# Kernel tuning notes

Measured on AMD Instinct MI355X. Metric: run time of the kernel, lower is better.

## Reference

```python
import jax, jax.numpy as jnp
import numpy as np

HIDDEN_DIM = 1024
HEAD_DIM = 64


def setup_inputs() -> dict:
    key = jax.random.key(0)
    kx, kq, kk, kv, ko = jax.random.split(key, 5)
    B, S = 4, 4096
    x = jax.random.normal(kx, (B, S, HIDDEN_DIM), dtype=jnp.float32)
    # nn.Linear(in, out, bias=False) weight has shape [out, in]; y = x @ W.T
    scale = 1.0 / np.sqrt(HIDDEN_DIM)
    Wq = jax.random.normal(kq, (HEAD_DIM, HIDDEN_DIM), dtype=jnp.float32) * scale
    Wk = jax.random.normal(kk, (HEAD_DIM, HIDDEN_DIM), dtype=jnp.float32) * scale
    Wv = jax.random.normal(kv, (HEAD_DIM, HIDDEN_DIM), dtype=jnp.float32) * scale
    Wo = jax.random.normal(ko, (HIDDEN_DIM, HEAD_DIM), dtype=jnp.float32) * (1.0 / np.sqrt(HEAD_DIM))
    return {"x": x, "Wq": Wq, "Wk": Wk, "Wv": Wv, "Wo": Wo}


def reference(x, Wq, Wk, Wv, Wo):
    # projections: x [B,S,H] @ W.T [H,D] -> [B,S,D]
    q = jnp.einsum('bsh,dh->bsd', x, Wq)
    k = jnp.einsum('bsh,dh->bsd', x, Wk)
    v = jnp.einsum('bsh,dh->bsd', x, Wv)
    d = q.shape[-1]
    scores = jnp.einsum('bqd,bkd->bqk', q, k) / jnp.sqrt(jnp.asarray(d, q.dtype))
    S = q.shape[1]
    causal_mask = jnp.triu(jnp.ones((S, S), dtype=bool), k=1)  # True above diagonal
    scores = jnp.where(causal_mask[None, :, :], jnp.asarray(-jnp.inf, scores.dtype), scores)
    attn = jax.nn.softmax(scores, axis=-1)
    out = jnp.einsum('bqk,bkd->bqd', attn, v)
    return jnp.einsum('bsd,hd->bsh', out, Wo)
```

## Files before the change

kernel.cpp:

```cpp
#include <hip/hip_runtime.h>
#include <hip/hip_bf16.h>


typedef __attribute__((ext_vector_type(8))) __bf16 bf16x8;
typedef __attribute__((ext_vector_type(4))) float f32x4;

#define BATCH 4
#define SEQ   4096
#define HID   1024
#define HDIM  64
#define CHT   8
#define NCMAX 8

__device__ __forceinline__ unsigned short f2bf(float f) {
  unsigned u = __builtin_bit_cast(unsigned, f);
  u += 0x7fffu + ((u >> 16) & 1u);
  return (unsigned short)(u >> 16);
}
__device__ __forceinline__ float bf2f(unsigned short u) {
  unsigned v = ((unsigned)u) << 16;
  return __builtin_bit_cast(float, v);
}
__device__ __forceinline__ __bf16 f2bf16(float f) {
  unsigned short us = f2bf(f);
  return __builtin_bit_cast(__bf16, us);
}
__device__ __forceinline__ bf16x8 cvt8(const float* __restrict__ p) {
  f32x4 a = *reinterpret_cast<const f32x4*>(p);
  f32x4 b = *reinterpret_cast<const f32x4*>(p + 4);
  bf16x8 r;
  r[0] = f2bf16(a[0]); r[1] = f2bf16(a[1]); r[2] = f2bf16(a[2]); r[3] = f2bf16(a[3]);
  r[4] = f2bf16(b[0]); r[5] = f2bf16(b[1]); r[6] = f2bf16(b[2]); r[7] = f2bf16(b[3]);
  return r;
}

__global__ __launch_bounds__(256) void convert_w(
    const float* __restrict__ Wq, const float* __restrict__ Wk,
    const float* __restrict__ Wv, const float* __restrict__ Wo,
    unsigned short* __restrict__ q, unsigned short* __restrict__ k,
    unsigned short* __restrict__ v, unsigned short* __restrict__ o) {
  const int gid = blockIdx.x * 256 + threadIdx.x;
  const int mat = gid >> 16, idx = gid & 0xFFFF;
  const float* s = (mat == 0) ? Wq : (mat == 1) ? Wk : (mat == 2) ? Wv : Wo;
  unsigned short* d = (mat == 0) ? q : (mat == 1) ? k : (mat == 2) ? v : o;
  d[idx] = f2bf(s[idx]);
}

__global__ __launch_bounds__(256) void qkv_proj(
    const float* __restrict__ x,
    const unsigned short* __restrict__ Wqb,
    const unsigned short* __restrict__ Wkb,
    const unsigned short* __restrict__ Wvb,
    unsigned short* __restrict__ Q,
    unsigned short* __restrict__ K,
    unsigned short* __restrict__ Vt) {
  const int z    = blockIdx.x;
  const int mb   = blockIdx.y;
  const int lane = threadIdx.x & 63;
  const int wave = threadIdx.x >> 6;
  const int quad = lane >> 4;
  const int l15  = lane & 15;
  const int row0 = mb * 64 + wave * 16;

  const unsigned short* W = (z == 0) ? Wqb : (z == 1) ? Wkb : Wvb;

  f32x4 acc[4];
  const f32x4 zero = {0.f, 0.f, 0.f, 0.f};
#pragma unroll
  for (int n = 0; n < 4; ++n) acc[n] = zero;

  const float* ap = x + (size_t)(row0 + l15) * HID + quad * 8;
  for (int kk = 0; kk < HID; kk += 32) {
    bf16x8 a = cvt8(ap + kk);
#pragma unroll
    for (int n = 0; n < 4; ++n) {
      bf16x8 b = *reinterpret_cast<const bf16x8*>(W + (size_t)(n * 16 + l15) * HID + kk + quad * 8);
      acc[n] = __builtin_amdgcn_mfma_f32_16x16x32_bf16(a, b, acc[n], 0, 0, 0);
    }
  }

  if (z < 2) {
    unsigned short* Out = (z == 0) ? Q : K;
#pragma unroll
    for (int n = 0; n < 4; ++n)
#pragma unroll
      for (int r = 0; r < 4; ++r) {
        const int row = row0 + quad * 4 + r;
        const int col = n * 16 + l15;
        Out[(size_t)row * HDIM + col] = f2bf(acc[n][r]);
      }
  } else {
#pragma unroll
    for (int n = 0; n < 4; ++n)
#pragma unroll
      for (int r = 0; r < 4; ++r) {
        const int row = row0 + quad * 4 + r;
        const int col = n * 16 + l15;
        const int bb = row >> 12, sl = row & 4095;
        Vt[(size_t)bb * HDIM * SEQ + (size_t)col * SEQ + sl] = f2bf(acc[n][r]);
      }
  }
}

#define LSTR 72

__global__ __launch_bounds__(256) void flash_splitk(
    const unsigned short* __restrict__ Qg,
    const unsigned short* __restrict__ Kg,
    const unsigned short* __restrict__ Vt,
    unsigned short* __restrict__ Og,
    unsigned short* __restrict__ Opart,
    float2* __restrict__ Ml) {
  const int qb = blockIdx.x;
  const int b  = blockIdx.y;
  const int c  = blockIdx.z;
  const int nc = (qb >> 3) + 1;
  if (c >= nc) return;
  const int j0 = c * CHT;
  const int j1 = min(j0 + CHT, qb + 1);

  const int tid  = threadIdx.x;
  const int lane = tid & 63;
  const int wave = tid >> 6;
  const int quad = lane >> 4;
  const int l15  = lane & 15;

  __shared__ unsigned short kt[64 * LSTR];
  __shared__ unsigned short vt[64 * LSTR];
  __shared__ unsigned short pt[4][16 * LSTR];

  const size_t base  = (size_t)b * SEQ * HDIM;
  const size_t baseT = (size_t)b * HDIM * SEQ;
  const int qrow0 = qb * 64 + wave * 16;

  bf16x8 aq[2];
  {
    const unsigned short* qp = Qg + base + (size_t)(qrow0 + l15) * HDIM + quad * 8;
    aq[0] = *reinterpret_cast<const bf16x8*>(qp);
    aq[1] = *reinterpret_cast<const bf16x8*>(qp + 32);
  }

  f32x4 o[4];
  const f32x4 zero = {0.f, 0.f, 0.f, 0.f};
#pragma unroll
  for (int n = 0; n < 4; ++n) o[n] = zero;
  float m_i[4], l_i[4];
#pragma unroll
  for (int r = 0; r < 4; ++r) { m_i[r] = -__builtin_inff(); l_i[r] = 0.f; }

  unsigned short* pw = pt[wave];
  const int srow = tid >> 2, sc0 = (tid & 3) * 16;
  const unsigned short* kb = Kg + base;
  const unsigned short* vb = Vt + baseT;

  const float C = 0.125f * 1.44269504f;

  uint4 pk0, pk1, pv0, pv1;
  {
    const uint4* kp = reinterpret_cast<const uint4*>(kb + (size_t)(j0 * 64 + srow) * HDIM + sc0);
    pk0 = kp[0]; pk1 = kp[1];
    const uint4* vp = reinterpret_cast<const uint4*>(vb + (size_t)srow * SEQ + j0 * 64 + sc0);
    pv0 = vp[0]; pv1 = vp[1];
    *reinterpret_cast<uint4*>(&kt[srow * LSTR + sc0])     = pk0;
    *reinterpret_cast<uint4*>(&kt[srow * LSTR + sc0 + 8]) = pk1;
    *reinterpret_cast<uint4*>(&vt[srow * LSTR + sc0])     = pv0;
    *reinterpret_cast<uint4*>(&vt[srow * LSTR + sc0 + 8]) = pv1;
  }

  for (int j = j0; j < j1; ++j) {
    __syncthreads();
    const bool pre = (j + 1 < j1);
    if (pre) {
      const uint4* kp = reinterpret_cast<const uint4*>(kb + (size_t)((j + 1) * 64 + srow) * HDIM + sc0);
      pk0 = kp[0]; pk1 = kp[1];
      const uint4* vp = reinterpret_cast<const uint4*>(vb + (size_t)srow * SEQ + (j + 1) * 64 + sc0);
      pv0 = vp[0]; pv1 = vp[1];
    }

    f32x4 s[4];
#pragma unroll
    for (int n = 0; n < 4; ++n) s[n] = zero;
#pragma unroll
    for (int ks = 0; ks < 2; ++ks) {
#pragma unroll
      for (int n = 0; n < 4; ++n) {
        bf16x8 bk = *reinterpret_cast<const bf16x8*>(&kt[(n * 16 + l15) * LSTR + ks * 32 + quad * 8]);
        s[n] = __builtin_amdgcn_mfma_f32_16x16x32_bf16(aq[ks], bk, s[n], 0, 0, 0);
      }
    }

    if (j == qb) {
#pragma unroll
      for (int n = 0; n < 4; ++n) {
        const int col = n * 16 + l15;
#pragma unroll
        for (int r = 0; r < 4; ++r) {
          const int rowl = wave * 16 + quad * 4 + r;
          if (col > rowl) s[n][r] = -__builtin_inff();
        }
      }
    }

    float mnew[4], alpha[4], mC[4];
#pragma unroll
    for (int r = 0; r < 4; ++r) {
      float v = fmaxf(fmaxf(s[0][r], s[1][r]), fmaxf(s[2][r], s[3][r]));
#pragma unroll
      for (int off = 1; off < 16; off <<= 1) v = fmaxf(v, __shfl_xor(v, off, 64));
      mnew[r]  = fmaxf(m_i[r], v);
      alpha[r] = __builtin_amdgcn_exp2f((m_i[r] - mnew[r]) * C);
      mC[r]    = mnew[r] * C;
    }
    float p[4][4];
#pragma unroll
    for (int n = 0; n < 4; ++n)
#pragma unroll
      for (int r = 0; r < 4; ++r)
        p[n][r] = __builtin_amdgcn_exp2f(__builtin_fmaf(s[n][r], C, -mC[r]));
#pragma unroll
    for (int r = 0; r < 4; ++r) {
      float v = (p[0][r] + p[1][r]) + (p[2][r] + p[3][r]);
#pragma unroll
      for (int off = 1; off < 16; off <<= 1) v += __shfl_xor(v, off, 64);
      l_i[r] = l_i[r] * alpha[r] + v;
      m_i[r] = mnew[r];
    }
#pragma unroll
    for (int n = 0; n < 4; ++n)
#pragma unroll
      for (int r = 0; r < 4; ++r) o[n][r] *= alpha[r];

#pragma unroll
    for (int n = 0; n < 4; ++n)
#pragma unroll
      for (int r = 0; r < 4; ++r)
        pw[(quad * 4 + r) * LSTR + n * 16 + l15] = f2bf(p[n][r]);

#pragma unroll
    for (int ks = 0; ks < 2; ++ks) {
      bf16x8 ap = *reinterpret_cast<const bf16x8*>(&pw[l15 * LSTR + ks * 32 + quad * 8]);
#pragma unroll
      for (int n = 0; n < 4; ++n) {
        bf16x8 bv = *reinterpret_cast<const bf16x8*>(&vt[(n * 16 + l15) * LSTR + ks * 32 + quad * 8]);
        o[n] = __builtin_amdgcn_mfma_f32_16x16x32_bf16(ap, bv, o[n], 0, 0, 0);
      }
    }

    __syncthreads();
    if (pre) {
      *reinterpret_cast<uint4*>(&kt[srow * LSTR + sc0])     = pk0;
      *reinterpret_cast<uint4*>(&kt[srow * LSTR + sc0 + 8]) = pk1;
      *reinterpret_cast<uint4*>(&vt[srow * LSTR + sc0])     = pv0;
      *reinterpret_cast<uint4*>(&vt[srow * LSTR + sc0 + 8]) = pv1;
    }
  }

  if (nc == 1) {
#pragma unroll
    for (int n = 0; n < 4; ++n)
#pragma unroll
      for (int r = 0; r < 4; ++r) {
        const int row = qrow0 + quad * 4 + r;
        const int col = n * 16 + l15;
        Og[base + (size_t)row * HDIM + col] = f2bf(o[n][r] / l_i[r]);
      }
  } else {
    const int slot = ((b * 64 + qb) << 3) + c;
#pragma unroll
    for (int n = 0; n < 4; ++n)
#pragma unroll
      for (int r = 0; r < 4; ++r) {
        const int rowl = wave * 16 + quad * 4 + r;
        const int col  = n * 16 + l15;
        Opart[(size_t)slot * 4096 + rowl * 64 + col] = f2bf(o[n][r]);
      }
    if (l15 == 0) {
#pragma unroll
      for (int r = 0; r < 4; ++r) {
        const int rowl = wave * 16 + quad * 4 + r;
        Ml[slot * 64 + rowl] = make_float2(m_i[r], l_i[r]);
      }
    }
  }
}

__global__ __launch_bounds__(256) void merge_splitk(
    const unsigned short* __restrict__ Opart,
    const float2* __restrict__ Ml,
    unsigned short* __restrict__ Og) {
  const int qb = blockIdx.x;
  if (qb < CHT) return;
  const int b  = blockIdx.y;
  const int nc = (qb >> 3) + 1;
  const int row = threadIdx.x >> 2;
  const int cg  = (threadIdx.x & 3) * 16;
  const int slot0 = (b * 64 + qb) << 3;

  float m[NCMAX], l[NCMAX];
  float M = -__builtin_inff();
  for (int c = 0; c < nc; ++c) {
    float2 ml = Ml[(slot0 + c) * 64 + row];
    m[c] = ml.x; l[c] = ml.y;
    M = fmaxf(M, m[c]);
  }
  const float C = 0.125f * 1.44269504f;
  float L = 0.f, acc[16];
#pragma unroll
  for (int i = 0; i < 16; ++i) acc[i] = 0.f;
  for (int c = 0; c < nc; ++c) {
    const float w = __builtin_amdgcn_exp2f((m[c] - M) * C);
    L += w * l[c];
    const unsigned short* p = Opart + (size_t)(slot0 + c) * 4096 + row * 64 + cg;
    uint4 u0 = *reinterpret_cast<const uint4*>(p);
    uint4 u1 = *reinterpret_cast<const uint4*>(p + 8);
    const unsigned* uu = &u0.x;
#pragma unroll
    for (int i = 0; i < 4; ++i) {
      acc[2 * i]     += w * bf2f((unsigned short)(uu[i] & 0xFFFF));
      acc[2 * i + 1] += w * bf2f((unsigned short)(uu[i] >> 16));
    }
    const unsigned* vv = &u1.x;
#pragma unroll
    for (int i = 0; i < 4; ++i) {
      acc[8 + 2 * i]     += w * bf2f((unsigned short)(vv[i] & 0xFFFF));
      acc[8 + 2 * i + 1] += w * bf2f((unsigned short)(vv[i] >> 16));
    }
  }
  const float inv = 1.f / L;
  uint4 o0, o1;
  unsigned* po = &o0.x;
#pragma unroll
  for (int i = 0; i < 4; ++i)
    po[i] = (unsigned)f2bf(acc[2 * i] * inv) | ((unsigned)f2bf(acc[2 * i + 1] * inv) << 16);
  unsigned* p1 = &o1.x;
#pragma unroll
  for (int i = 0; i < 4; ++i)
    p1[i] = (unsigned)f2bf(acc[8 + 2 * i] * inv) | ((unsigned)f2bf(acc[8 + 2 * i + 1] * inv) << 16);
  unsigned short* dst = Og + (size_t)b * SEQ * HDIM + (size_t)(qb * 64 + row) * HDIM + cg;
  *reinterpret_cast<uint4*>(dst)     = o0;
  *reinterpret_cast<uint4*>(dst + 8) = o1;
}

__global__ __launch_bounds__(256) void out_proj(
    const unsigned short* __restrict__ O,
    const unsigned short* __restrict__ Wob,
    float* __restrict__ Y) {
  const int nb   = blockIdx.x;
  const int mb   = blockIdx.y;
  const int lane = threadIdx.x & 63;
  const int wave = threadIdx.x >> 6;
  const int quad = lane >> 4;
  const int l15  = lane & 15;
  const int row0 = mb * 64 + wave * 16;

  f32x4 acc[4];
  const f32x4 zero = {0.f, 0.f, 0.f, 0.f};
#pragma unroll
  for (int n = 0; n < 4; ++n) acc[n] = zero;

  const unsigned short* op = O + (size_t)(row0 + l15) * HDIM + quad * 8;
  bf16x8 a0 = *reinterpret_cast<const bf16x8*>(op);
  bf16x8 a1 = *reinterpret_cast<const bf16x8*>(op + 32);
#pragma unroll
  for (int n = 0; n < 4; ++n) {
    const int col = nb * 64 + n * 16 + l15;
    const unsigned short* wp = Wob + (size_t)col * HDIM + quad * 8;
    bf16x8 b0 = *reinterpret_cast<const bf16x8*>(wp);
    bf16x8 b1 = *reinterpret_cast<const bf16x8*>(wp + 32);
    acc[n] = __builtin_amdgcn_mfma_f32_16x16x32_bf16(a0, b0, acc[n], 0, 0, 0);
    acc[n] = __builtin_amdgcn_mfma_f32_16x16x32_bf16(a1, b1, acc[n], 0, 0, 0);
  }
#pragma unroll
  for (int n = 0; n < 4; ++n)
#pragma unroll
    for (int r = 0; r < 4; ++r) {
      const int row = row0 + quad * 4 + r;
      const int col = nb * 64 + n * 16 + l15;
      Y[(size_t)row * HID + col] = acc[n][r];
    }
}

extern "C" void kernel_launch(void* const* d_in, const int* in_sizes, int n_in,
                              void* d_out, int out_size, void* d_ws, size_t ws_size,
                              hipStream_t stream) {
  const float* x  = (const float*)d_in[0];
  const float* Wq = (const float*)d_in[1];
  const float* Wk = (const float*)d_in[2];
  const float* Wv = (const float*)d_in[3];
  const float* Wo = (const float*)d_in[4];
  float* Y = (float*)d_out;

  const size_t qkv_elems = (size_t)BATCH * SEQ * HDIM;
  const size_t w_elems   = (size_t)HDIM * HID;
  unsigned short* Q     = (unsigned short*)d_ws;
  unsigned short* K     = Q + qkv_elems;
  unsigned short* Vt    = K + qkv_elems;
  unsigned short* O     = Vt + qkv_elems;
  unsigned short* Wqb   = O + qkv_elems;
  unsigned short* Wkb   = Wqb + w_elems;
  unsigned short* Wvb   = Wkb + w_elems;
  unsigned short* Wob   = Wvb + w_elems;
  unsigned short* Opart = Wob + w_elems;
  float2*         Ml    = (float2*)(Opart + (size_t)2048 * 4096);

  convert_w   <<<1024,               256, 0, stream>>>(Wq, Wk, Wv, Wo, Wqb, Wkb, Wvb, Wob);
  qkv_proj    <<<dim3(3, 256),       256, 0, stream>>>(x, Wqb, Wkb, Wvb, Q, K, Vt);
  flash_splitk<<<dim3(64, 4, NCMAX), 256, 0, stream>>>(Q, K, Vt, O, Opart, Ml);
  merge_splitk<<<dim3(64, 4),        256, 0, stream>>>(Opart, Ml, O);
  out_proj    <<<dim3(16, 256),      256, 0, stream>>>(O, Wob, Y);
}
```

Baseline: 239.5 us.

## Fuse Q/K/V projections per wave so x is read once, with prefetch

```diff
diff --git a/kernel.cpp b/kernel.cpp
--- a/kernel.cpp
+++ b/kernel.cpp
@@ -25,9 +25,7 @@
   unsigned short us = f2bf(f);
   return __builtin_bit_cast(__bf16, us);
 }
-__device__ __forceinline__ bf16x8 cvt8(const float* __restrict__ p) {
-  f32x4 a = *reinterpret_cast<const f32x4*>(p);
-  f32x4 b = *reinterpret_cast<const f32x4*>(p + 4);
+__device__ __forceinline__ bf16x8 pack8(f32x4 a, f32x4 b) {
   bf16x8 r;
   r[0] = f2bf16(a[0]); r[1] = f2bf16(a[1]); r[2] = f2bf16(a[2]); r[3] = f2bf16(a[3]);
   r[4] = f2bf16(b[0]); r[5] = f2bf16(b[1]); r[6] = f2bf16(b[2]); r[7] = f2bf16(b[3]);
@@ -46,7 +44,7 @@
   d[idx] = f2bf(s[idx]);
 }
 
-__global__ __launch_bounds__(256) void qkv_proj(
+__global__ __launch_bounds__(64) void qkv_proj(
     const float* __restrict__ x,
     const unsigned short* __restrict__ Wqb,
     const unsigned short* __restrict__ Wkb,
@@ -54,32 +52,48 @@
     unsigned short* __restrict__ Q,
     unsigned short* __restrict__ K,
     unsigned short* __restrict__ Vt) {
-  const int z    = blockIdx.x;
-  const int mb   = blockIdx.y;
-  const int lane = threadIdx.x & 63;
-  const int wave = threadIdx.x >> 6;
+  const int mb   = blockIdx.x;
+  const int lane = threadIdx.x;
   const int quad = lane >> 4;
   const int l15  = lane & 15;
-  const int row0 = mb * 64 + wave * 16;
-
-  const unsigned short* W = (z == 0) ? Wqb : (z == 1) ? Wkb : Wvb;
-
-  f32x4 acc[4];
+  const int row0 = mb * 16;
+
+  const unsigned short* Ws[3] = {Wqb, Wkb, Wvb};
+
+  f32x4 acc[3][4];
   const f32x4 zero = {0.f, 0.f, 0.f, 0.f};
 #pragma unroll
-  for (int n = 0; n < 4; ++n) acc[n] = zero;
+  for (int z = 0; z < 3; ++z)
+#pragma unroll
+    for (int n = 0; n < 4; ++n) acc[z][n] = zero;
 
   const float* ap = x + (size_t)(row0 + l15) * HID + quad * 8;
+
+  f32x4 af[2][2];
+  af[0][0] = *reinterpret_cast<const f32x4*>(ap);
+  af[0][1] = *reinterpret_cast<const f32x4*>(ap + 4);
+  af[1][0] = *reinterpret_cast<const f32x4*>(ap + 32);
+  af[1][1] = *reinterpret_cast<const f32x4*>(ap + 36);
+
+  int slot = 0;
   for (int kk = 0; kk < HID; kk += 32) {
-    bf16x8 a = cvt8(ap + kk);
-#pragma unroll
-    for (int n = 0; n < 4; ++n) {
-      bf16x8 b = *reinterpret_cast<const bf16x8*>(W + (size_t)(n * 16 + l15) * HID + kk + quad * 8);
-      acc[n] = __builtin_amdgcn_mfma_f32_16x16x32_bf16(a, b, acc[n], 0, 0, 0);
-    }
-  }
-
-  if (z < 2) {
+    bf16x8 a = pack8(af[slot][0], af[slot][1]);
+    if (kk + 64 < HID) {
+      af[slot][0] = *reinterpret_cast<const f32x4*>(ap + kk + 64);
+      af[slot][1] = *reinterpret_cast<const f32x4*>(ap + kk + 68);
+    }
+    slot ^= 1;
+#pragma unroll
+    for (int z = 0; z < 3; ++z)
+#pragma unroll
+      for (int n = 0; n < 4; ++n) {
+        bf16x8 b = *reinterpret_cast<const bf16x8*>(Ws[z] + (size_t)(n * 16 + l15) * HID + kk + quad * 8);
+        acc[z][n] = __builtin_amdgcn_mfma_f32_16x16x32_bf16(a, b, acc[z][n], 0, 0, 0);
+      }
+  }
+
+#pragma unroll
+  for (int z = 0; z < 2; ++z) {
     unsigned short* Out = (z == 0) ? Q : K;
 #pragma unroll
     for (int n = 0; n < 4; ++n)
@@ -87,19 +101,18 @@
       for (int r = 0; r < 4; ++r) {
         const int row = row0 + quad * 4 + r;
         const int col = n * 16 + l15;
-        Out[(size_t)row * HDIM + col] = f2bf(acc[n][r]);
-      }
-  } else {
-#pragma unroll
-    for (int n = 0; n < 4; ++n)
-#pragma unroll
-      for (int r = 0; r < 4; ++r) {
-        const int row = row0 + quad * 4 + r;
-        const int col = n * 16 + l15;
-        const int bb = row >> 12, sl = row & 4095;
-        Vt[(size_t)bb * HDIM * SEQ + (size_t)col * SEQ + sl] = f2bf(acc[n][r]);
-      }
-  }
+        Out[(size_t)row * HDIM + col] = f2bf(acc[z][n][r]);
+      }
+  }
+#pragma unroll
+  for (int n = 0; n < 4; ++n)
+#pragma unroll
+    for (int r = 0; r < 4; ++r) {
+      const int row = row0 + quad * 4 + r;
+      const int col = n * 16 + l15;
+      const int bb = row >> 12, sl = row & 4095;
+      Vt[(size_t)bb * HDIM * SEQ + (size_t)col * SEQ + sl] = f2bf(acc[2][n][r]);
+    }
 }
 
 #define LSTR 72
@@ -404,7 +417,7 @@
   float2*         Ml    = (float2*)(Opart + (size_t)2048 * 4096);
 
   convert_w   <<<1024,               256, 0, stream>>>(Wq, Wk, Wv, Wo, Wqb, Wkb, Wvb, Wob);
-  qkv_proj    <<<dim3(3, 256),       256, 0, stream>>>(x, Wqb, Wkb, Wvb, Q, K, Vt);
+  qkv_proj    <<<1024,                64, 0, stream>>>(x, Wqb, Wkb, Wvb, Q, K, Vt);
   flash_splitk<<<dim3(64, 4, NCMAX), 256, 0, stream>>>(Q, K, Vt, O, Opart, Ml);
   merge_splitk<<<dim3(64, 4),        256, 0, stream>>>(Opart, Ml, O);
   out_proj    <<<dim3(16, 256),      256, 0, stream>>>(O, Wob, Y);
```

After: 244.2 us. No clear change (+1.9%).
